# Kernel optimization log

Measured on AMD Instinct MI355X. Metric: run time of the kernel, lower is better.

The kernel has to match this reference:

```python
import jax, jax.numpy as jnp
import numpy as np

SIG_G = [1, 1, 1]          # Clifford signature Cl(3,0): 2^3 = 8 blades
N_BLADES = 1 << len(SIG_G)
LAYER_DIMS = [256, 512, 256]
BATCH = 64
ALPHA = 0.1


def _cayley(g):
    """Cayley table C[a,b,k]: e_a * e_b = C[a,b,a^b] * e_{a^b} (blades as bitmasks)."""
    n = len(g)
    K = 1 << n
    C = np.zeros((K, K, K), dtype=np.float32)
    for a in range(K):
        for b in range(K):
            # canonical reordering sign: count generator swaps
            s, aa = 0, a >> 1
            while aa:
                s += bin(aa & b).count('1')
                aa >>= 1
            sign = -1.0 if (s & 1) else 1.0
            # metric contraction for repeated generators
            for i in range(n):
                if (a >> i) & 1 and (b >> i) & 1:
                    sign *= g[i]
            C[a, b, a ^ b] = sign
    return C


def _reverse_signs(n):
    """Reversion sign per blade: (-1)^{r(r-1)/2} for grade r."""
    K = 1 << n
    r = np.array([bin(k).count('1') for k in range(K)])
    return ((-1.0) ** (r * (r - 1) // 2)).astype(np.float32)


CAYLEY = jnp.asarray(_cayley(SIG_G))          # (K, K, K), sparse signed table
REV = jnp.asarray(_reverse_signs(len(SIG_G)))  # (K,)


def geometric_product(A, W, C):
    # A: (B, N, K) multivectors, W: (M, N, K) multivector weights -> (B, M, K)
    # out[b,m,k] = sum_n sum_{a,c} C[a,c,k] * A[b,n,a] * W[m,n,c]
    return jnp.einsum('bna,mnc,ack->bmk', A, W, C)


def setup_inputs() -> dict:
    key = jax.random.key(0)
    k_x, k_w1, k_w2 = jax.random.split(key, 3)
    x = jax.random.normal(k_x, (BATCH, LAYER_DIMS[0], N_BLADES), dtype=jnp.float32)
    w1 = jax.random.normal(k_w1, (LAYER_DIMS[0], LAYER_DIMS[1], N_BLADES), dtype=jnp.float32) * 0.1
    w2 = jax.random.normal(k_w2, (LAYER_DIMS[1], LAYER_DIMS[2], N_BLADES), dtype=jnp.float32) * 0.1
    return {"x": x, "w1": w1, "w2": w2, "n_iter": 20}


def reference(x, w1, w2, n_iter):
    ws = [w1, w2]
    B = x.shape[0]
    # states[0] is detached input (x.detach().clone() in torch)
    states = [jax.lax.stop_gradient(x)]
    for w in ws:
        states.append(jnp.zeros((B, w.shape[1], N_BLADES), dtype=x.dtype))
    for _ in range(n_iter):
        for l in range(1, len(states)):
            w = ws[l - 1]
            x_hat = geometric_product(states[l], w, CAYLEY)          # (B, D_{l-1}, K)
            err = states[l - 1] - x_hat
            w_T = jnp.transpose(w * REV, (1, 0, 2))                  # reverse + transpose
            # torch: grad = -gp(err, w_T); states[l] -= alpha*grad  => += alpha*gp
            states[l] = states[l] + ALPHA * geometric_product(err, w_T, CAYLEY)
    return tuple(states)
```

## Files before the change

kernel.cpp:

```cpp
#include <hip/hip_runtime.h>

typedef unsigned short u16;
typedef __attribute__((ext_vector_type(4))) float f32x4;
typedef __attribute__((ext_vector_type(8))) __bf16 bf16x8;
typedef __attribute__((ext_vector_type(8))) u16 u16x8;

#define ALPHA_F 0.1f

__device__ __host__ constexpr bool SGN(int a, int c) {
  return ((((c & 1) & (((a >> 1) ^ (a >> 2)) & 1)) ^
           (((c >> 1) & 1) & ((a >> 2) & 1))) != 0);
}
__device__ __host__ constexpr float REVF(int c) {
  const int r = (c & 1) + ((c >> 1) & 1) + ((c >> 2) & 1);
  return (r >= 2) ? -1.f : 1.f;
}
__device__ __forceinline__ u16 bf_rnd(float f) {
  unsigned u = __float_as_uint(f);
  return (u16)((u + 0x7FFFu + ((u >> 16) & 1u)) >> 16);
}
__device__ __forceinline__ float bf_val(u16 h) {
  return __uint_as_float(((unsigned)h) << 16);
}
__device__ __forceinline__ f32x4 mf(bf16x8 a, bf16x8 b, f32x4 c) {
  return __builtin_amdgcn_mfma_f32_16x16x32_bf16(a, b, c, 0, 0, 0);
}
__device__ __forceinline__ bf16x8 negf(bf16x8 v) {
  u16x8 u = __builtin_bit_cast(u16x8, v);
  const u16x8 m = {0x8000, 0x8000, 0x8000, 0x8000, 0x8000, 0x8000, 0x8000, 0x8000};
  u = u ^ m;
  return __builtin_bit_cast(bf16x8, u);
}

__global__ __launch_bounds__(256) void pack_in(
    const float* __restrict__ x, const float* __restrict__ w1,
    const float* __restrict__ w2, u16* P1h, u16* P1l, u16* Q1, u16* Qc1,
    u16* P2h, u16* P2l, u16* Q2, u16* Axh, u16* Axl, u16* Vpk2,
    u16* BpAh, u16* BpAl, u16* Z0h, u16* Z0l, float* out0) {
  const int t = blockIdx.x * 256 + threadIdx.x;
  if (t < 131072) {
    const int cc = t & 511;
    const int ro = (t >> 9) & 31;
    const int c = t >> 14;
    u16 h1[8], l1[8], hc[8], lc[8];
#pragma unroll
    for (int e = 0; e < 8; ++e) {
      const int r = ro * 8 + e;
      const float v = w1[((size_t)r * 512 + cc) * 8 + c];
      const float q1 = REVF(c) * v;
      const u16 hh = bf_rnd(q1);
      h1[e] = hh;
      l1[e] = bf_rnd(q1 - bf_val(hh));
      const float qc = ALPHA_F * q1;
      const u16 hh2 = bf_rnd(qc);
      hc[e] = hh2;
      lc[e] = bf_rnd(qc - bf_val(hh2));
    }
    const size_t qrun = (size_t)((cc >> 4) * 2 + (ro >> 4)) * 32768 +
                        ((ro >> 2) & 3) * 512 + (ro & 3) * 128 +
                        (cc & 15) * 8 + (size_t)c * 4096;
    *(u16x8*)&Q1[qrun] = *(u16x8*)h1;
    *(u16x8*)&Q1[qrun + 2048] = *(u16x8*)l1;
    *(u16x8*)&Qc1[qrun] = *(u16x8*)hc;
    *(u16x8*)&Qc1[qrun + 2048] = *(u16x8*)lc;
  } else if (t < 262144) {
    const int u = t - 131072;
    const int c2 = u & 255;
    const int ro = (u >> 8) & 63;
    const int c = u >> 14;
    u16 h2[8], l2[8], hw[8], lw[8];
#pragma unroll
    for (int e = 0; e < 8; ++e) {
      const int r = ro * 8 + e;
      const float v = w2[((size_t)r * 256 + c2) * 8 + c];
      const float q2 = REVF(c) * v;
      const u16 hh = bf_rnd(q2);
      h2[e] = hh;
      l2[e] = bf_rnd(q2 - bf_val(hh));
      const float qw = ALPHA_F * q2;
      const u16 hh2 = bf_rnd(qw);
      hw[e] = hh2;
      lw[e] = bf_rnd(qw - bf_val(hh2));
    }
    const size_t tail = ((ro >> 2) & 3) * 512 + (ro & 3) * 128 +
                        (c2 & 15) * 8 + (size_t)c * 4096;
    const size_t qo = (size_t)((c2 >> 4) * 4 + (ro >> 4)) * 32768 + tail;
    const size_t wo = (size_t)((c2 >> 4) * 6 + 2 + (ro >> 4)) * 32768 + tail;
    *(u16x8*)&Q2[qo] = *(u16x8*)h2;
    *(u16x8*)&Q2[qo + 2048] = *(u16x8*)l2;
    *(u16x8*)&Vpk2[wo] = *(u16x8*)hw;
    *(u16x8*)&Vpk2[wo + 2048] = *(u16x8*)lw;
#pragma unroll
    for (int e = 0; e < 8; ++e) {
      const int r = ro * 8 + e;
      const size_t bo = ((size_t)(c * 32 + (c2 >> 3)) * 512 + r) * 8 + (c2 & 7);
      BpAh[bo] = hw[e];
      BpAl[bo] = lw[e];
    }
  } else if (t < 393216) {
    const int u = t - 262144;
    const int cc = u & 511;
    const int ro = (u >> 9) & 31;
    const int a = u >> 14;
    u16 hh[8], ll[8];
#pragma unroll
    for (int e = 0; e < 8; ++e) {
      const int r = ro * 8 + e;
      const float v = w1[((size_t)r * 512 + cc) * 8 + a];
      const u16 h = bf_rnd(v);
      hh[e] = h;
      ll[e] = bf_rnd(v - bf_val(h));
    }
    const size_t o = ((size_t)(a * 32 + ro) * 512 + cc) * 8;
    *(u16x8*)&P1h[o] = *(u16x8*)hh;
    *(u16x8*)&P1l[o] = *(u16x8*)ll;
  } else if (t < 524288) {
    const int u = t - 393216;
    const int c2 = u & 255;
    const int ro = (u >> 8) & 63;
    const int a = u >> 14;
    u16 hh[8], ll[8];
#pragma unroll
    for (int e = 0; e < 8; ++e) {
      const int r = ro * 8 + e;
      const float v = w2[((size_t)r * 256 + c2) * 8 + a];
      const u16 h = bf_rnd(v);
      hh[e] = h;
      ll[e] = bf_rnd(v - bf_val(h));
    }
    const size_t o = ((size_t)(a * 64 + ro) * 256 + c2) * 8;
    *(u16x8*)&P2h[o] = *(u16x8*)hh;
    *(u16x8*)&P2l[o] = *(u16x8*)ll;
  } else if (t < 540672) {
    const int u = t - 524288;
    const int b = u & 63;
    const int no = (u >> 6) & 31;
    const int a = u >> 11;
    u16 hh[8], ll[8];
#pragma unroll
    for (int e = 0; e < 8; ++e) {
      const int n = no * 8 + e;
      const float v = x[((size_t)b * 256 + n) * 8 + a];
      const u16 h = bf_rnd(v);
      hh[e] = h;
      ll[e] = bf_rnd(v - bf_val(h));
    }
    const size_t o = ((size_t)(a * 32 + no) * 64 + b) * 8;
    *(u16x8*)&Axh[o] = *(u16x8*)hh;
    *(u16x8*)&Axl[o] = *(u16x8*)ll;
  } else if (t < 573440) {
    const int u = t - 540672;
    ((float4*)out0)[u] = ((const float4*)x)[u];
  } else if (t < 606208) {
    const int u = t - 573440;
    const int hl = u >> 14, i = u & 16383;
    const int a = i >> 11, j = i & 2047;
    const u16x8 z = {0, 0, 0, 0, 0, 0, 0, 0};
    u16* Z = hl ? Z0l : Z0h;
    *(u16x8*)&Z[(size_t)a * 49152 + (size_t)j * 8] = z;
  }
}

__global__ __launch_bounds__(512) void composeK(
    const u16* __restrict__ P1h, const u16* __restrict__ P1l,
    const u16* __restrict__ Q1, const u16* __restrict__ P2h,
    const u16* __restrict__ P2l, const u16* __restrict__ Q2,
    const u16* __restrict__ Axh, const u16* __restrict__ Axl,
    const u16* __restrict__ Qc1, u16* Vpk1, u16* Vpk2,
    u16* V1pAh, u16* V1pAl, u16* UpAh, u16* UpAl,
    u16* Z0h, u16* Z0l, float* c1Z) {
  __shared__ float pan[8][2176];

  const int bid = blockIdx.x, tid = threadIdx.x;
  const int w = tid >> 6, l = tid & 63;
  const int lg = l >> 4, lm = l & 15;

  if (bid < 640) {
    const bool isU = bid < 128;
    const int p = isU ? (bid >> 3) : ((bid - 128) >> 4);
    const int rq = isU ? (bid & 7) : ((bid - 128) & 15);
    const int row0 = rq * 32 + lm, row1 = row0 + 16;
    const int NWf = isU ? 2 : 1;
    const int slmul = isU ? 4 : 2;
    const int KCf = isU ? 64 : 32;
    const int NROWf = isU ? 256 : 512;
    const u16* Vb = isU ? Q2 : Q1;
    const u16* Aph = isU ? P2h : P1h;
    const u16* Apl = isU ? P2l : P1l;

    f32x4 acc0[8], acc1[8];
#pragma unroll
    for (int k = 0; k < 8; ++k) {
      acc0[k] = f32x4{0.f, 0.f, 0.f, 0.f};
      acc1[k] = f32x4{0.f, 0.f, 0.f, 0.f};
    }
    for (int wi = 0; wi < NWf; ++wi) {
      const int n0 = w * (NWf * 32) + wi * 32;
      const int sl = n0 >> 7, hst = (n0 >> 5) & 3;
      const u16* Vimg = Vb + ((size_t)(p * slmul + sl) << 15) + hst * 512 +
                        lg * 128 + lm * 8;
      const int kc = (n0 >> 3) + lg;
      bf16x8 a0h[8], a0l[8], a1h[8], a1l[8];
#pragma unroll
      for (int a = 0; a < 8; ++a) {
        const size_t o0 = ((size_t)(a * KCf + kc) * NROWf + row0) * 8;
        const size_t o1 = ((size_t)(a * KCf + kc) * NROWf + row1) * 8;
        a0h[a] = *(const bf16x8*)(Aph + o0);
        a0l[a] = *(const bf16x8*)(Apl + o0);
        a1h[a] = *(const bf16x8*)(Aph + o1);
        a1l[a] = *(const bf16x8*)(Apl + o1);
      }
      __builtin_amdgcn_s_setprio(1);
#pragma unroll
      for (int c = 0; c < 8; ++c) {
        const bf16x8 vhp = *(const bf16x8*)(Vimg + (size_t)c * 4096);
        const bf16x8 vlp = *(const bf16x8*)(Vimg + (size_t)c * 4096 + 2048);
        const bf16x8 vhn = negf(vhp), vln = negf(vlp);
#pragma unroll
        for (int a = 0; a < 8; ++a) {
          const int k = a ^ c;
          const bf16x8 vh = SGN(a, c) ? vhn : vhp;
          const bf16x8 vl = SGN(a, c) ? vln : vlp;
          acc0[k] = mf(a0h[a], vh, acc0[k]);
          acc0[k] = mf(a0l[a], vh, acc0[k]);
          acc0[k] = mf(a0h[a], vl, acc0[k]);
          acc1[k] = mf(a1h[a], vh, acc1[k]);
          acc1[k] = mf(a1l[a], vh, acc1[k]);
          acc1[k] = mf(a1h[a], vl, acc1[k]);
        }
      }
      __builtin_amdgcn_s_setprio(0);
    }
#pragma unroll
    for (int rg = 0; rg < 2; ++rg) {
#pragma unroll
      for (int k = 0; k < 8; ++k)
#pragma unroll
        for (int q = 0; q < 4; ++q)
          pan[w][(k * 16 + lg * 4 + q) * 17 + lm] =
              rg ? acc1[k][q] : acc0[k][q];
      __syncthreads();
      if (tid < 256) {
        const int k = tid >> 5, rw = (tid >> 1) & 15, ch = tid & 1;
        const int boff = (k * 16 + rw) * 17 + ch * 8;
        f32x4 s0 = {0.f, 0.f, 0.f, 0.f}, s1 = {0.f, 0.f, 0.f, 0.f};
        for (int ss = 0; ss < 8; ++ss) {
          s0 += *(const f32x4*)&pan[ss][boff];
          s1 += *(const f32x4*)&pan[ss][boff + 4];
        }
        float v[8];
#pragma unroll
        for (int e = 0; e < 4; ++e) { v[e] = s0[e]; v[4 + e] = s1[e]; }
        const int n = rq * 32 + rg * 16 + rw;

        u16* base = isU ? Vpk2 : Vpk1;
        const int blk = (isU ? p * 6 : p * 4) + (n >> 7);
        u16* d = base + ((size_t)blk << 15) + (size_t)k * 4096 +
                 ((n >> 5) & 3) * 512 + ((n >> 3) & 3) * 128 + (n & 7);
        u16 ph[8], pl[8];
#pragma unroll
        for (int e = 0; e < 8; ++e) {
          const int m = p * 16 + ch * 8 + e;
          const float val =
              ((k == 0) && (n == m) ? 1.0f : 0.0f) - ALPHA_F * v[e];
          const u16 hh = bf_rnd(val);
          const u16 ll = bf_rnd(val - bf_val(hh));
          d[(size_t)(ch * 8 + e) * 8] = hh;
          d[2048 + (size_t)(ch * 8 + e) * 8] = ll;
          ph[e] = hh;
          pl[e] = ll;
        }
        if (isU) {
          const size_t po = (((size_t)k * 32 + p * 2 + ch) * 256 + n) * 8;
          *(u16x8*)&UpAh[po] = *(u16x8*)ph;
          *(u16x8*)&UpAl[po] = *(u16x8*)pl;
        } else {
          const size_t po = (((size_t)k * 64 + p * 2 + ch) * 512 + n) * 8;
          *(u16x8*)&V1pAh[po] = *(u16x8*)ph;
          *(u16x8*)&V1pAl[po] = *(u16x8*)pl;
        }
      }
      __syncthreads();
    }
    return;
  }

  {
    const int idx = bid - 640;
    const int rb = idx & 3, p = idx >> 2;
    const int row = rb * 16 + lm;

    f32x4 acc[8];
#pragma unroll
    for (int k = 0; k < 8; ++k) acc[k] = f32x4{0.f, 0.f, 0.f, 0.f};

    const int n0 = w * 32;
    const int sl = n0 >> 7, hst = (n0 >> 5) & 3;
    const u16* Vimg = Qc1 + ((size_t)(p * 2 + sl) << 15) + hst * 512 +
                      lg * 128 + lm * 8;
    const int kc = (n0 >> 3) + lg;
    bf16x8 ah[8], al[8];
#pragma unroll
    for (int a = 0; a < 8; ++a) {
      const size_t o = ((size_t)(a * 32 + kc) * 64 + row) * 8;
      ah[a] = *(const bf16x8*)(Axh + o);
      al[a] = *(const bf16x8*)(Axl + o);
    }
    __builtin_amdgcn_s_setprio(1);
#pragma unroll
    for (int c = 0; c < 8; ++c) {
      const bf16x8 vhp = *(const bf16x8*)(Vimg + (size_t)c * 4096);
      const bf16x8 vlp = *(const bf16x8*)(Vimg + (size_t)c * 4096 + 2048);
      const bf16x8 vhn = negf(vhp), vln = negf(vlp);
#pragma unroll
      for (int a = 0; a < 8; ++a) {
        const int k = a ^ c;
        const bf16x8 vh = SGN(a, c) ? vhn : vhp;
        const bf16x8 vl = SGN(a, c) ? vln : vlp;
        acc[k] = mf(ah[a], vh, acc[k]);
        acc[k] = mf(al[a], vh, acc[k]);
        acc[k] = mf(ah[a], vl, acc[k]);
      }
    }
    __builtin_amdgcn_s_setprio(0);

#pragma unroll
    for (int k = 0; k < 8; ++k)
#pragma unroll
      for (int q = 0; q < 4; ++q)
        pan[w][(k * 16 + lg * 4 + q) * 17 + lm] = acc[k][q];
    __syncthreads();

    if (tid < 256) {
      const int k = tid >> 5, rw = (tid >> 1) & 15, ch = tid & 1;
      const int boff = (k * 16 + rw) * 17 + ch * 8;
      f32x4 s0 = {0.f, 0.f, 0.f, 0.f}, s1 = {0.f, 0.f, 0.f, 0.f};
      for (int ss = 0; ss < 8; ++ss) {
        s0 += *(const f32x4*)&pan[ss][boff];
        s1 += *(const f32x4*)&pan[ss][boff + 4];
      }
      float v[8];
#pragma unroll
      for (int e = 0; e < 4; ++e) { v[e] = s0[e]; v[4 + e] = s1[e]; }
      const int b = rb * 16 + rw;
      float* cp_ = c1Z + (((size_t)k * 64 + p * 2 + ch) * 64 + b) * 8;
      u16x8 h8, l8;
#pragma unroll
      for (int e = 0; e < 8; ++e) {
        cp_[e] = v[e];
        const u16 hh = bf_rnd(v[e]);
        h8[e] = hh;
        l8[e] = bf_rnd(v[e] - bf_val(hh));
      }
      const size_t zo = (((size_t)k * 96 + 32 + p * 2 + ch) * 64 + b) * 8;
      *(u16x8*)&Z0h[zo] = h8;
      *(u16x8*)&Z0l[zo] = l8;
    }
  }
}

struct IArgs {
  const u16 *Zch, *Zcl;
  u16 *Znh, *Znl;
  const u16 *V1, *V2;
  const float *add1, *add2;
  float *oa1, *oa2;
  float *out1, *out2;
  int n_g1;
};

template <bool G1>
__device__ __forceinline__ void iter_body(const IArgs& A, int vbid, int t18,
                                          int fin, float (*pan)[2176]) {
  const int tid = threadIdx.x;
  const int w = tid >> 6, l = tid & 63;
  const int lg = l >> 4, lm = l & 15;
  const int rb = G1 ? vbid : vbid - A.n_g1;
  constexpr int NPAN = G1 ? 32 : 16;
  const int p = rb & (NPAN - 1);
  const int bh = rb / NPAN;
  const int b0 = bh * 16;
  constexpr int KW = G1 ? 64 : 96;
  constexpr int NW = G1 ? 2 : 3;
  constexpr int acb0 = G1 ? 32 : 0;
  constexpr int slmul = G1 ? 4 : 6;
  const u16* Vb = G1 ? A.V1 : A.V2;

  f32x4 acc[8];
#pragma unroll
  for (int k = 0; k < 8; ++k) acc[k] = f32x4{0.f, 0.f, 0.f, 0.f};

#pragma unroll
  for (int wi = 0; wi < NW; ++wi) {
    const int n0 = w * KW + wi * 32;
    const int sl = n0 >> 7, hst = (n0 >> 5) & 3;
    const u16* Vimg = Vb + ((size_t)(p * slmul + sl) << 15) + hst * 512 +
                      lg * 128 + lm * 8;
    const size_t ao = ((size_t)(acb0 + (n0 >> 3) + lg) * 64 + b0 + lm) * 8;
    bf16x8 ah[8], al[8];
#pragma unroll
    for (int a = 0; a < 8; ++a) {
      ah[a] = *(const bf16x8*)(A.Zch + (size_t)a * 49152 + ao);
      al[a] = *(const bf16x8*)(A.Zcl + (size_t)a * 49152 + ao);
    }
    __builtin_amdgcn_s_setprio(1);
#pragma unroll
    for (int c = 0; c < 8; ++c) {
      const bf16x8 vhp = *(const bf16x8*)(Vimg + (size_t)c * 4096);
      const bf16x8 vlp = *(const bf16x8*)(Vimg + (size_t)c * 4096 + 2048);
      const bf16x8 vhn = negf(vhp), vln = negf(vlp);
#pragma unroll
      for (int a = 0; a < 8; ++a) {
        const int k = a ^ c;
        const bf16x8 vh = SGN(a, c) ? vhn : vhp;
        const bf16x8 vl = SGN(a, c) ? vln : vlp;
        acc[k] = mf(ah[a], vh, acc[k]);
        acc[k] = mf(al[a], vh, acc[k]);
        acc[k] = mf(ah[a], vl, acc[k]);
      }
    }
    __builtin_amdgcn_s_setprio(0);
  }

#pragma unroll
  for (int k = 0; k < 8; ++k)
#pragma unroll
    for (int q = 0; q < 4; ++q)
      pan[w][(k * 16 + lg * 4 + q) * 17 + lm] = acc[k][q];
  __syncthreads();

  if (tid < 256) {
    const int k = tid >> 5, row = (tid >> 1) & 15, ch = tid & 1;
    const int boff = (k * 16 + row) * 17 + ch * 8;
    f32x4 s0 = {0.f, 0.f, 0.f, 0.f}, s1 = {0.f, 0.f, 0.f, 0.f};
    for (int ss = 0; ss < 8; ++ss) {
      s0 += *(const f32x4*)&pan[ss][boff];
      s1 += *(const f32x4*)&pan[ss][boff + 4];
    }
    const int b = b0 + row;
    if constexpr (G1) {
      if (A.add1) {
        const float* ca = A.add1 + (((size_t)k * 64 + p * 2 + ch) * 64 + b) * 8;
        s0 += *(const f32x4*)ca;
        s1 += *(const f32x4*)(ca + 4);
      }
    } else {
      if (A.add2) {
        const float* ca = A.add2 + (((size_t)k * 32 + p * 2 + ch) * 64 + b) * 8;
        s0 += *(const f32x4*)ca;
        s1 += *(const f32x4*)(ca + 4);
      }
    }
    float v[8];
#pragma unroll
    for (int e = 0; e < 4; ++e) { v[e] = s0[e]; v[4 + e] = s1[e]; }
    if constexpr (G1) {
      if (A.oa1) {
        float* q = A.oa1 + (((size_t)k * 64 + p * 2 + ch) * 64 + b) * 8;
#pragma unroll
        for (int e = 0; e < 8; ++e) q[e] = v[e];
      }
    } else {
      if (A.oa2) {
        float* q = A.oa2 + (((size_t)k * 32 + p * 2 + ch) * 64 + b) * 8;
#pragma unroll
        for (int e = 0; e < 8; ++e) q[e] = v[e];
      }
    }
    if (!fin) {
      u16x8 h8, l8;
#pragma unroll
      for (int e = 0; e < 8; ++e) {
        const u16 hh = bf_rnd(v[e]);
        h8[e] = hh;
        l8[e] = bf_rnd(v[e] - bf_val(hh));
      }
      const size_t zo =
          (((size_t)k * 96 + (G1 ? 32 : 0) + p * 2 + ch) * 64 + b) * 8;
      *(u16x8*)&A.Znh[zo] = h8;
      *(u16x8*)&A.Znl[zo] = l8;
    }
    if constexpr (G1) {
      if (t18) {
#pragma unroll
        for (int e = 0; e < 8; ++e)
          A.out1[((size_t)b * 512 + p * 16 + ch * 8 + e) * 8 + k] = v[e];
      }
    } else {
      if (fin) {
#pragma unroll
        for (int e = 0; e < 8; ++e)
          A.out2[((size_t)b * 256 + p * 16 + ch * 8 + e) * 8 + k] = v[e];
      }
    }
  }
}

__global__ __launch_bounds__(512, 2) void iter_k(IArgs A, int t18, int fin) {
  __shared__ float pan[8][2176];
  if ((int)blockIdx.x < A.n_g1) iter_body<true>(A, blockIdx.x, t18, fin, pan);
  else iter_body<false>(A, blockIdx.x, t18, fin, pan);
}

struct C2A {
  const u16 *V1pAh, *V1pAl, *UpAh, *UpAl, *BpAh, *BpAl;
  const u16 *Vpk1, *Wcat;
  u16 *V1sqI, *Wcat2;
};

__global__ __launch_bounds__(512) void combo(IArgs S, C2A C) {
  __shared__ float pan[8][2176];
  const int bid = blockIdx.x, tid = threadIdx.x;

  if (bid < 192) {
    if (bid < S.n_g1) iter_body<true>(S, bid, 0, 0, pan);
    else iter_body<false>(S, bid, 0, 0, pan);
    return;
  }
  const int cb = bid - 192;
  const int w = tid >> 6, l = tid & 63;
  const int lg = l >> 4, lm = l & 15;

  if (cb < 512) {
    const int p = cb >> 4, rq = cb & 15;
    const int row0 = rq * 32 + lm, row1 = row0 + 16;
    f32x4 acc0[8], acc1[8];
#pragma unroll
    for (int k = 0; k < 8; ++k) {
      acc0[k] = f32x4{0.f, 0.f, 0.f, 0.f};
      acc1[k] = f32x4{0.f, 0.f, 0.f, 0.f};
    }
#pragma unroll
    for (int wi = 0; wi < 2; ++wi) {
      const int g = w * 2 + wi;
      const u16* Vimg = C.Vpk1 + ((size_t)(p * 4 + (g >> 2)) << 15) +
                        (g & 3) * 512 + lg * 128 + lm * 8;
      const int kc = g * 4 + lg;
      bf16x8 a0h[8], a0l[8], a1h[8], a1l[8];
#pragma unroll
      for (int a = 0; a < 8; ++a) {
        const size_t o0 = ((size_t)(a * 64 + kc) * 512 + row0) * 8;
        const size_t o1 = ((size_t)(a * 64 + kc) * 512 + row1) * 8;
        a0h[a] = *(const bf16x8*)(C.V1pAh + o0);
        a0l[a] = *(const bf16x8*)(C.V1pAl + o0);
        a1h[a] = *(const bf16x8*)(C.V1pAh + o1);
        a1l[a] = *(const bf16x8*)(C.V1pAl + o1);
      }
      __builtin_amdgcn_s_setprio(1);
#pragma unroll
      for (int c = 0; c < 8; ++c) {
        const bf16x8 vhp = *(const bf16x8*)(Vimg + (size_t)c * 4096);
        const bf16x8 vlp = *(const bf16x8*)(Vimg + (size_t)c * 4096 + 2048);
        const bf16x8 vhn = negf(vhp), vln = negf(vlp);
#pragma unroll
        for (int a = 0; a < 8; ++a) {
          const int k = a ^ c;
          const bf16x8 vh = SGN(a, c) ? vhn : vhp;
          const bf16x8 vl = SGN(a, c) ? vln : vlp;
          acc0[k] = mf(a0h[a], vh, acc0[k]);
          acc0[k] = mf(a0l[a], vh, acc0[k]);
          acc0[k] = mf(a0h[a], vl, acc0[k]);
          acc1[k] = mf(a1h[a], vh, acc1[k]);
          acc1[k] = mf(a1l[a], vh, acc1[k]);
          acc1[k] = mf(a1h[a], vl, acc1[k]);
        }
      }
      __builtin_amdgcn_s_setprio(0);
    }
#pragma unroll
    for (int rg = 0; rg < 2; ++rg) {
#pragma unroll
      for (int k = 0; k < 8; ++k)
#pragma unroll
        for (int q = 0; q < 4; ++q)
          pan[w][(k * 16 + lg * 4 + q) * 17 + lm] =
              rg ? acc1[k][q] : acc0[k][q];
      __syncthreads();
      if (tid < 256) {
        const int k = tid >> 5, rw = (tid >> 1) & 15, ch = tid & 1;
        const int boff = (k * 16 + rw) * 17 + ch * 8;
        f32x4 s0 = {0.f, 0.f, 0.f, 0.f}, s1 = {0.f, 0.f, 0.f, 0.f};
        for (int ss = 0; ss < 8; ++ss) {
          s0 += *(const f32x4*)&pan[ss][boff];
          s1 += *(const f32x4*)&pan[ss][boff + 4];
        }
        float v[8];
#pragma unroll
        for (int e = 0; e < 4; ++e) { v[e] = s0[e]; v[4 + e] = s1[e]; }
        const int n = rq * 32 + rg * 16 + rw;
        const int blk = p * 4 + (n >> 7);
        u16* d = C.V1sqI + ((size_t)blk << 15) + (size_t)k * 4096 +
                 ((n >> 5) & 3) * 512 + ((n >> 3) & 3) * 128 + (n & 7);
#pragma unroll
        for (int e = 0; e < 8; ++e) {
          const float val = v[e];
          const u16 hh = bf_rnd(val);
          d[(size_t)(ch * 8 + e) * 8] = hh;
          d[2048 + (size_t)(ch * 8 + e) * 8] = bf_rnd(val - bf_val(hh));
        }
      }
      __syncthreads();
    }
    return;
  }

  int seg, rb, p;
  if (cb < 1024) { seg = 1; rb = (cb - 512) & 31; p = (cb - 512) >> 5; }
  else { seg = 2; rb = (cb - 1024) & 15; p = (cb - 1024) >> 4; }
  const int nwin = seg == 1 ? 3 : 1;
  const int row = rb * 16 + lm;

  f32x4 acc[8];
#pragma unroll
  for (int k = 0; k < 8; ++k) acc[k] = f32x4{0.f, 0.f, 0.f, 0.f};

  for (int wi = 0; wi < nwin; ++wi) {
    const int g = w * nwin + wi;
    const u16 *Aph, *Apl;
    int AKC, AR, kcb;
    const u16* Vimg;
    if (seg == 1) {
      if (g < 8) {
        Aph = C.BpAh; Apl = C.BpAl; AKC = 32; AR = 512; kcb = g * 4;
        Vimg = C.Wcat + ((size_t)(p * 6 + (g >> 2)) << 15) + (g & 3) * 512;
      } else {
        const int g2_ = g - 8;
        Aph = C.V1pAh; Apl = C.V1pAl; AKC = 64; AR = 512; kcb = g2_ * 4;
        Vimg = C.Wcat + ((size_t)(p * 6 + 2 + (g2_ >> 2)) << 15) + (g2_ & 3) * 512;
      }
    } else {
      Aph = C.UpAh; Apl = C.UpAl; AKC = 32; AR = 256; kcb = g * 4;
      Vimg = C.Wcat + ((size_t)(p * 6 + (g >> 2)) << 15) + (g & 3) * 512;
    }
    Vimg += lg * 128 + lm * 8;
    const int kc = kcb + lg;
    bf16x8 ah[8], al[8];
#pragma unroll
    for (int a = 0; a < 8; ++a) {
      const size_t o = ((size_t)(a * AKC + kc) * AR + row) * 8;
      ah[a] = *(const bf16x8*)(Aph + o);
      al[a] = *(const bf16x8*)(Apl + o);
    }
    __builtin_amdgcn_s_setprio(1);
#pragma unroll
    for (int c = 0; c < 8; ++c) {
      const bf16x8 vhp = *(const bf16x8*)(Vimg + (size_t)c * 4096);
      const bf16x8 vlp = *(const bf16x8*)(Vimg + (size_t)c * 4096 + 2048);
      const bf16x8 vhn = negf(vhp), vln = negf(vlp);
#pragma unroll
      for (int a = 0; a < 8; ++a) {
        const int k = a ^ c;
        const bf16x8 vh = SGN(a, c) ? vhn : vhp;
        const bf16x8 vl = SGN(a, c) ? vln : vlp;
        acc[k] = mf(ah[a], vh, acc[k]);
        acc[k] = mf(al[a], vh, acc[k]);
        acc[k] = mf(ah[a], vl, acc[k]);
      }
    }
    __builtin_amdgcn_s_setprio(0);
  }

#pragma unroll
  for (int k = 0; k < 8; ++k)
#pragma unroll
    for (int q = 0; q < 4; ++q)
      pan[w][(k * 16 + lg * 4 + q) * 17 + lm] = acc[k][q];
  __syncthreads();

  if (tid < 256) {
    const int k = tid >> 5, rw = (tid >> 1) & 15, ch = tid & 1;
    const int boff = (k * 16 + rw) * 17 + ch * 8;
    f32x4 s0 = {0.f, 0.f, 0.f, 0.f}, s1 = {0.f, 0.f, 0.f, 0.f};
    for (int ss = 0; ss < 8; ++ss) {
      s0 += *(const f32x4*)&pan[ss][boff];
      s1 += *(const f32x4*)&pan[ss][boff + 4];
    }
    float v[8];
#pragma unroll
    for (int e = 0; e < 4; ++e) { v[e] = s0[e]; v[4 + e] = s1[e]; }
    const int n = rb * 16 + rw;

    const int blk = seg == 1 ? (p * 6 + 2 + (n >> 7)) : (p * 6 + (n >> 7));
    u16* d = C.Wcat2 + ((size_t)blk << 15) + (size_t)k * 4096 +
             ((n >> 5) & 3) * 512 + ((n >> 3) & 3) * 128 + (n & 7);
#pragma unroll
    for (int e = 0; e < 8; ++e) {
      const float val = v[e];
      const u16 hh = bf_rnd(val);
      d[(size_t)(ch * 8 + e) * 8] = hh;
      d[2048 + (size_t)(ch * 8 + e) * 8] = bf_rnd(val - bf_val(hh));
    }
  }
}

extern "C" void kernel_launch(void* const* d_in, const int* in_sizes, int n_in,
                              void* d_out, int out_size, void* d_ws,
                              size_t ws_size, hipStream_t stream) {
  const float* x = (const float*)d_in[0];
  const float* w1 = (const float*)d_in[1];
  const float* w2 = (const float*)d_in[2];

  float* out0 = (float*)d_out;
  float* out1 = out0 + 131072;
  float* out2 = out1 + 262144;

  char* W = (char*)d_ws;
  const size_t MB = 1ull << 20;
  u16* Vpk1 = (u16*)(W);
  u16* Wcat = (u16*)(W + 8 * MB);
  u16* Q1 = (u16*)(W + 14 * MB);
  u16* Q2 = (u16*)(W + 18 * MB);
  u16* Qc1 = (u16*)(W + 22 * MB);
  u16* P1h = (u16*)(W + 26 * MB);
  u16* P1l = (u16*)(W + 28 * MB);
  u16* P2h = (u16*)(W + 30 * MB);
  u16* P2l = (u16*)(W + 32 * MB);
  u16* Axh = (u16*)(W + 34 * MB);
  u16* Axl = (u16*)(W + 34 * MB + 262144);
  float* c1Z = (float*)(W + 35 * MB);
  u16* V1sqI = (u16*)(W + 36 * MB);
  u16* Wcat2 = (u16*)(W + 44 * MB);
  u16* V1pAh = (u16*)(W + 50 * MB);
  u16* V1pAl = (u16*)(W + 54 * MB);
  u16* UpAh = (u16*)(W + 58 * MB);
  u16* UpAl = (u16*)(W + 59 * MB);
  u16* BpAh = (u16*)(W + 60 * MB);
  u16* BpAl = (u16*)(W + 62 * MB);
  float* c1bZ = (float*)(W + 64 * MB);
  float* d2Z = (float*)(W + 65 * MB);
  u16* Z0h = (u16*)(W + 66 * MB);
  u16* Z0l = Z0h + 393216;
  u16* Z1h = Z0h + 786432;
  u16* Z1l = Z0h + 1179648;

  pack_in<<<2368, 256, 0, stream>>>(x, w1, w2, P1h, P1l, Q1, Qc1, P2h, P2l, Q2,
                                    Axh, Axl, Wcat, BpAh, BpAl, Z0h, Z0l, out0);

  composeK<<<768, 512, 0, stream>>>(P1h, P1l, Q1, P2h, P2l, Q2, Axh, Axl, Qc1,
                                    Vpk1, Wcat, V1pAh, V1pAl, UpAh, UpAl,
                                    Z0h, Z0l, c1Z);

  {
    IArgs seed{Z0h, Z0l, Z1h, Z1l, Vpk1, Wcat, c1Z, nullptr,
               c1bZ, d2Z, out1, out2, 128};
    C2A c2{V1pAh, V1pAl, UpAh, UpAl, BpAh, BpAl, Vpk1, Wcat, V1sqI, Wcat2};
    combo<<<1472, 512, 0, stream>>>(seed, c2);
  }

  for (int tau = 0; tau < 9; ++tau) {
    const bool odd = tau & 1;
    IArgs ia{odd ? Z0h : Z1h, odd ? Z0l : Z1l,
             odd ? Z1h : Z0h, odd ? Z1l : Z0l,
             V1sqI, Wcat2, c1bZ, d2Z, nullptr, nullptr, out1, out2, 128};
    iter_k<<<192, 512, 0, stream>>>(ia, tau == 8 ? 1 : 0, 0);
  }

  {
    IArgs ia{Z0h, Z0l, Z1h, Z1l, Vpk1, Wcat, nullptr, nullptr,
             nullptr, nullptr, out1, out2, 0};
    iter_k<<<64, 512, 0, stream>>>(ia, 0, 1);
  }
}
```

Measured before the change: 322.7 us.

## Hoist weight-image loads ahead of MFMA loops and double-buffer A fragments

Weight fragment loads that used to sit inside the MFMA loop are now issued in batches into registers before the compute loops run. In the main iteration kernel, the next A-slice fragments are prefetched into a second register set while the current slice is computed, giving software pipelining across the up to three weight slices. The launch bound drops the two-blocks-per-CU minimum so the compiler may use the extra registers. This aims to hide global-load latency behind MFMA work, at the risk of lower occupancy and higher register pressure.

```diff
diff --git a/kernel.cpp b/kernel.cpp
--- a/kernel.cpp
+++ b/kernel.cpp
@@ -210,26 +210,36 @@
         a1h[a] = *(const bf16x8*)(Aph + o1);
         a1l[a] = *(const bf16x8*)(Apl + o1);
       }
-      __builtin_amdgcn_s_setprio(1);
-#pragma unroll
-      for (int c = 0; c < 8; ++c) {
-        const bf16x8 vhp = *(const bf16x8*)(Vimg + (size_t)c * 4096);
-        const bf16x8 vlp = *(const bf16x8*)(Vimg + (size_t)c * 4096 + 2048);
-        const bf16x8 vhn = negf(vhp), vln = negf(vlp);
-#pragma unroll
-        for (int a = 0; a < 8; ++a) {
-          const int k = a ^ c;
-          const bf16x8 vh = SGN(a, c) ? vhn : vhp;
-          const bf16x8 vl = SGN(a, c) ? vln : vlp;
-          acc0[k] = mf(a0h[a], vh, acc0[k]);
-          acc0[k] = mf(a0l[a], vh, acc0[k]);
-          acc0[k] = mf(a0h[a], vl, acc0[k]);
-          acc1[k] = mf(a1h[a], vh, acc1[k]);
-          acc1[k] = mf(a1l[a], vh, acc1[k]);
-          acc1[k] = mf(a1h[a], vl, acc1[k]);
+#pragma unroll
+      for (int half = 0; half < 2; ++half) {
+        bf16x8 vh4[4], vl4[4];
+#pragma unroll
+        for (int cq = 0; cq < 4; ++cq) {
+          vh4[cq] = *(const bf16x8*)(Vimg + (size_t)(half * 4 + cq) * 4096);
+          vl4[cq] =
+              *(const bf16x8*)(Vimg + (size_t)(half * 4 + cq) * 4096 + 2048);
         }
-      }
-      __builtin_amdgcn_s_setprio(0);
+        __builtin_amdgcn_s_setprio(1);
+#pragma unroll
+        for (int cq = 0; cq < 4; ++cq) {
+          const int c = half * 4 + cq;
+          const bf16x8 vhp = vh4[cq], vlp = vl4[cq];
+          const bf16x8 vhn = negf(vhp), vln = negf(vlp);
+#pragma unroll
+          for (int a = 0; a < 8; ++a) {
+            const int k = a ^ c;
+            const bf16x8 vh = SGN(a, c) ? vhn : vhp;
+            const bf16x8 vl = SGN(a, c) ? vln : vlp;
+            acc0[k] = mf(a0h[a], vh, acc0[k]);
+            acc0[k] = mf(a0l[a], vh, acc0[k]);
+            acc0[k] = mf(a0h[a], vl, acc0[k]);
+            acc1[k] = mf(a1h[a], vh, acc1[k]);
+            acc1[k] = mf(a1l[a], vh, acc1[k]);
+            acc1[k] = mf(a1h[a], vl, acc1[k]);
+          }
+        }
+        __builtin_amdgcn_s_setprio(0);
+      }
     }
 #pragma unroll
     for (int rg = 0; rg < 2; ++rg) {
@@ -299,18 +309,22 @@
     const u16* Vimg = Qc1 + ((size_t)(p * 2 + sl) << 15) + hst * 512 +
                       lg * 128 + lm * 8;
     const int kc = (n0 >> 3) + lg;
-    bf16x8 ah[8], al[8];
+    bf16x8 ah[8], al[8], vh8[8], vl8[8];
 #pragma unroll
     for (int a = 0; a < 8; ++a) {
       const size_t o = ((size_t)(a * 32 + kc) * 64 + row) * 8;
       ah[a] = *(const bf16x8*)(Axh + o);
       al[a] = *(const bf16x8*)(Axl + o);
     }
+#pragma unroll
+    for (int c = 0; c < 8; ++c) {
+      vh8[c] = *(const bf16x8*)(Vimg + (size_t)c * 4096);
+      vl8[c] = *(const bf16x8*)(Vimg + (size_t)c * 4096 + 2048);
+    }
     __builtin_amdgcn_s_setprio(1);
 #pragma unroll
     for (int c = 0; c < 8; ++c) {
-      const bf16x8 vhp = *(const bf16x8*)(Vimg + (size_t)c * 4096);
-      const bf16x8 vlp = *(const bf16x8*)(Vimg + (size_t)c * 4096 + 2048);
+      const bf16x8 vhp = vh8[c], vlp = vl8[c];
       const bf16x8 vhn = negf(vhp), vln = negf(vlp);
 #pragma unroll
       for (int a = 0; a < 8; ++a) {
@@ -390,36 +404,59 @@
 #pragma unroll
   for (int k = 0; k < 8; ++k) acc[k] = f32x4{0.f, 0.f, 0.f, 0.f};
 
-#pragma unroll
-  for (int wi = 0; wi < NW; ++wi) {
+  auto LOADA = [&](int wi, bf16x8* h, bf16x8* lo) {
+    const int n0 = w * KW + wi * 32;
+    const size_t ao = ((size_t)(acb0 + (n0 >> 3) + lg) * 64 + b0 + lm) * 8;
+#pragma unroll
+    for (int a = 0; a < 8; ++a) {
+      h[a] = *(const bf16x8*)(A.Zch + (size_t)a * 49152 + ao);
+      lo[a] = *(const bf16x8*)(A.Zcl + (size_t)a * 49152 + ao);
+    }
+  };
+  auto LOADV = [&](int wi, bf16x8* vhv, bf16x8* vlv) {
     const int n0 = w * KW + wi * 32;
     const int sl = n0 >> 7, hst = (n0 >> 5) & 3;
     const u16* Vimg = Vb + ((size_t)(p * slmul + sl) << 15) + hst * 512 +
                       lg * 128 + lm * 8;
-    const size_t ao = ((size_t)(acb0 + (n0 >> 3) + lg) * 64 + b0 + lm) * 8;
-    bf16x8 ah[8], al[8];
-#pragma unroll
-    for (int a = 0; a < 8; ++a) {
-      ah[a] = *(const bf16x8*)(A.Zch + (size_t)a * 49152 + ao);
-      al[a] = *(const bf16x8*)(A.Zcl + (size_t)a * 49152 + ao);
-    }
+#pragma unroll
+    for (int c = 0; c < 8; ++c) {
+      vhv[c] = *(const bf16x8*)(Vimg + (size_t)c * 4096);
+      vlv[c] = *(const bf16x8*)(Vimg + (size_t)c * 4096 + 2048);
+    }
+  };
+  auto COMP = [&](const bf16x8* h, const bf16x8* lo, const bf16x8* vhv,
+                  const bf16x8* vlv) {
     __builtin_amdgcn_s_setprio(1);
 #pragma unroll
     for (int c = 0; c < 8; ++c) {
-      const bf16x8 vhp = *(const bf16x8*)(Vimg + (size_t)c * 4096);
-      const bf16x8 vlp = *(const bf16x8*)(Vimg + (size_t)c * 4096 + 2048);
+      const bf16x8 vhp = vhv[c], vlp = vlv[c];
       const bf16x8 vhn = negf(vhp), vln = negf(vlp);
 #pragma unroll
       for (int a = 0; a < 8; ++a) {
         const int k = a ^ c;
         const bf16x8 vh = SGN(a, c) ? vhn : vhp;
         const bf16x8 vl = SGN(a, c) ? vln : vlp;
-        acc[k] = mf(ah[a], vh, acc[k]);
-        acc[k] = mf(al[a], vh, acc[k]);
-        acc[k] = mf(ah[a], vl, acc[k]);
+        acc[k] = mf(h[a], vh, acc[k]);
+        acc[k] = mf(lo[a], vh, acc[k]);
+        acc[k] = mf(h[a], vl, acc[k]);
       }
     }
     __builtin_amdgcn_s_setprio(0);
+  };
+
+  bf16x8 ah[8], al[8], ph[8], pl[8], vh8[8], vl8[8];
+  LOADA(0, ah, al);
+  LOADV(0, vh8, vl8);
+  if constexpr (NW > 1) LOADA(1, ph, pl);
+  COMP(ah, al, vh8, vl8);
+  if constexpr (NW > 1) {
+    LOADV(1, vh8, vl8);
+    if constexpr (NW > 2) LOADA(2, ah, al);
+    COMP(ph, pl, vh8, vl8);
+  }
+  if constexpr (NW > 2) {
+    LOADV(2, vh8, vl8);
+    COMP(ah, al, vh8, vl8);
   }
 
 #pragma unroll
@@ -496,7 +533,7 @@
   }
 }
 
-__global__ __launch_bounds__(512, 2) void iter_k(IArgs A, int t18, int fin) {
+__global__ __launch_bounds__(512) void iter_k(IArgs A, int t18, int fin) {
   __shared__ float pan[8][2176];
   if ((int)blockIdx.x < A.n_g1) iter_body<true>(A, blockIdx.x, t18, fin, pan);
   else iter_body<false>(A, blockIdx.x, t18, fin, pan);
@@ -546,26 +583,36 @@
         a1h[a] = *(const bf16x8*)(C.V1pAh + o1);
         a1l[a] = *(const bf16x8*)(C.V1pAl + o1);
       }
-      __builtin_amdgcn_s_setprio(1);
-#pragma unroll
-      for (int c = 0; c < 8; ++c) {
-        const bf16x8 vhp = *(const bf16x8*)(Vimg + (size_t)c * 4096);
-        const bf16x8 vlp = *(const bf16x8*)(Vimg + (size_t)c * 4096 + 2048);
-        const bf16x8 vhn = negf(vhp), vln = negf(vlp);
-#pragma unroll
-        for (int a = 0; a < 8; ++a) {
-          const int k = a ^ c;
-          const bf16x8 vh = SGN(a, c) ? vhn : vhp;
-          const bf16x8 vl = SGN(a, c) ? vln : vlp;
-          acc0[k] = mf(a0h[a], vh, acc0[k]);
-          acc0[k] = mf(a0l[a], vh, acc0[k]);
-          acc0[k] = mf(a0h[a], vl, acc0[k]);
-          acc1[k] = mf(a1h[a], vh, acc1[k]);
-          acc1[k] = mf(a1l[a], vh, acc1[k]);
-          acc1[k] = mf(a1h[a], vl, acc1[k]);
+#pragma unroll
+      for (int half = 0; half < 2; ++half) {
+        bf16x8 vh4[4], vl4[4];
+#pragma unroll
+        for (int cq = 0; cq < 4; ++cq) {
+          vh4[cq] = *(const bf16x8*)(Vimg + (size_t)(half * 4 + cq) * 4096);
+          vl4[cq] =
+              *(const bf16x8*)(Vimg + (size_t)(half * 4 + cq) * 4096 + 2048);
         }
-      }
-      __builtin_amdgcn_s_setprio(0);
+        __builtin_amdgcn_s_setprio(1);
+#pragma unroll
+        for (int cq = 0; cq < 4; ++cq) {
+          const int c = half * 4 + cq;
+          const bf16x8 vhp = vh4[cq], vlp = vl4[cq];
+          const bf16x8 vhn = negf(vhp), vln = negf(vlp);
+#pragma unroll
+          for (int a = 0; a < 8; ++a) {
+            const int k = a ^ c;
+            const bf16x8 vh = SGN(a, c) ? vhn : vhp;
+            const bf16x8 vl = SGN(a, c) ? vln : vlp;
+            acc0[k] = mf(a0h[a], vh, acc0[k]);
+            acc0[k] = mf(a0l[a], vh, acc0[k]);
+            acc0[k] = mf(a0h[a], vl, acc0[k]);
+            acc1[k] = mf(a1h[a], vh, acc1[k]);
+            acc1[k] = mf(a1l[a], vh, acc1[k]);
+            acc1[k] = mf(a1h[a], vl, acc1[k]);
+          }
+        }
+        __builtin_amdgcn_s_setprio(0);
+      }
     }
 #pragma unroll
     for (int rg = 0; rg < 2; ++rg) {
@@ -634,18 +681,22 @@
     }
     Vimg += lg * 128 + lm * 8;
     const int kc = kcb + lg;
-    bf16x8 ah[8], al[8];
+    bf16x8 ah[8], al[8], vh8[8], vl8[8];
 #pragma unroll
     for (int a = 0; a < 8; ++a) {
       const size_t o = ((size_t)(a * AKC + kc) * AR + row) * 8;
       ah[a] = *(const bf16x8*)(Aph + o);
       al[a] = *(const bf16x8*)(Apl + o);
     }
+#pragma unroll
+    for (int c = 0; c < 8; ++c) {
+      vh8[c] = *(const bf16x8*)(Vimg + (size_t)c * 4096);
+      vl8[c] = *(const bf16x8*)(Vimg + (size_t)c * 4096 + 2048);
+    }
     __builtin_amdgcn_s_setprio(1);
 #pragma unroll
     for (int c = 0; c < 8; ++c) {
-      const bf16x8 vhp = *(const bf16x8*)(Vimg + (size_t)c * 4096);
-      const bf16x8 vlp = *(const bf16x8*)(Vimg + (size_t)c * 4096 + 2048);
+      const bf16x8 vhp = vh8[c], vlp = vl8[c];
       const bf16x8 vhn = negf(vhp), vln = negf(vlp);
 #pragma unroll
       for (int a = 0; a < 8; ++a) {
```

Result: faster. 308.0 us (-4.6%).
